# Kernel optimization log

Measured on AMD Instinct MI355X. Metric: run time of the kernel, lower is better.

Reference implementation:

```python
import jax, jax.numpy as jnp
from jax import lax
import numpy as np

B, S_DEC, S_ENC = 32, 128, 128
V, E, H = 32000, 200, 128


def setup_inputs() -> dict:
    key = jax.random.key(0)
    ks = jax.random.split(key, 10)
    emb = jax.random.normal(ks[0], (V, E), dtype=jnp.float32)
    emb = emb.at[0].set(0.0)  # padding_idx row (char2id[' '] -> 0)
    return {
        "sequence": jax.random.randint(ks[1], (B, S_DEC), 0, V),
        "hs": jax.random.normal(ks[2], (B, S_ENC, H), dtype=jnp.float32),
        "h": jax.random.normal(ks[3], (1, B, H), dtype=jnp.float32),
        "emb": emb,
        "w_ih": jax.random.normal(ks[4], (3 * H, E), dtype=jnp.float32) * 0.05,
        "w_hh": jax.random.normal(ks[5], (3 * H, H), dtype=jnp.float32) * 0.05,
        "b_ih": jax.random.normal(ks[6], (3 * H,), dtype=jnp.float32) * 0.05,
        "b_hh": jax.random.normal(ks[7], (3 * H,), dtype=jnp.float32) * 0.05,
        "w_out": jax.random.normal(ks[8], (V, 2 * H), dtype=jnp.float32) * 0.05,
        "b_out": jax.random.normal(ks[9], (V,), dtype=jnp.float32) * 0.05,
    }


def _gru(x_gates, h0, w_hh, b_hh):
    # x_gates: [B, S, 3H] precomputed input projections; torch gate order r,z,n
    def step(hprev, xg):
        hg = hprev @ w_hh.T + b_hh
        xr, xz, xn = jnp.split(xg, 3, axis=-1)
        hr, hz, hn = jnp.split(hg, 3, axis=-1)
        r = jax.nn.sigmoid(xr + hr)
        z = jax.nn.sigmoid(xz + hz)
        n = jnp.tanh(xn + r * hn)
        hnew = (1.0 - z) * n + z * hprev
        return hnew, hnew

    hT, outs = lax.scan(step, h0, jnp.swapaxes(x_gates, 0, 1))  # scan over time
    return jnp.swapaxes(outs, 0, 1), hT  # [B,S,H], [B,H]


def reference(sequence, hs, h, emb, w_ih, w_hh, b_ih, b_hh, w_out, b_out):
    # Embedding lookup (padding row already zero)
    x = emb[sequence]  # [B, S_dec, E]
    x_gates = jnp.einsum("bse,ge->bsg", x, w_ih) + b_ih  # [B, S_dec, 3H]
    output, hT = _gru(x_gates, h[0], w_hh, b_hh)  # [B, S_dec, H]
    state = hT[None]  # [1, B, H]
    # s = bmm(hs, output^T): [B, S_enc, S_dec]; softmax over encoder axis (dim=1)
    s = jnp.einsum("beh,bdh->bed", hs, output)
    attention_weight = jax.nn.softmax(s, axis=1)
    # context: replaces the per-timestep python loop with one contraction
    c = jnp.einsum("bed,beh->bdh", attention_weight, hs)  # [B, S_dec, H]
    cat = jnp.concatenate([output, c], axis=-1)  # [B, S_dec, 2H]
    logits = jnp.einsum("bdh,vh->bdv", cat, w_out) + b_out  # [B, S_dec, V]
    return logits, state, attention_weight
```

## Files before the change

kernel.cpp:

```cpp
#include <hip/hip_runtime.h>
#include <hip/hip_bf16.h>

#define B_    32
#define SDEC  128
#define SENC  128
#define V_    32000
#define E_    200
#define H_    128
#define G3    384

typedef __attribute__((ext_vector_type(8))) short bf16x8;
typedef __attribute__((ext_vector_type(4))) float f32x4;
typedef __attribute__((ext_vector_type(2))) float f32x2;

#define GLOBAL_AS __attribute__((address_space(1)))
#define LDS_AS    __attribute__((address_space(3)))

__device__ __forceinline__ float fast_sigmoid(float x) {
  return 1.f / (1.f + __expf(-x));
}
__device__ __forceinline__ float fast_tanh(float x) {
  float e2 = __expf(2.f * x);
  return 1.f - 2.f / (e2 + 1.f);
}

__global__ __launch_bounds__(192) void k_embed_proj(
    const int* __restrict__ seq, const float* __restrict__ emb,
    const float* __restrict__ w_ih, const float* __restrict__ b_ih,
    float* __restrict__ xg) {
  __shared__ __align__(16) float xs[16][E_];
  __shared__ int sidx[16];
  const int r0 = blockIdx.x * 16;
  const int t = threadIdx.x;
  if (t < 16) sidx[t] = seq[r0 + t];
  __syncthreads();
  for (int i = t; i < 800; i += 192) {
    int r = i / 50, c = i - r * 50;
    *(float4*)&xs[r][c * 4] =
        *(const float4*)(emb + (size_t)sidx[r] * E_ + c * 4);
  }
  __syncthreads();
  const int g0 = t, g1 = t + 192;
  float a0[16], a1[16];
#pragma unroll
  for (int r = 0; r < 16; r++) { a0[r] = 0.f; a1[r] = 0.f; }
  const float* w0 = w_ih + (size_t)g0 * E_;
  const float* w1 = w_ih + (size_t)g1 * E_;
  for (int k = 0; k < E_; k += 4) {
    float4 wv0 = *(const float4*)(w0 + k);
    float4 wv1 = *(const float4*)(w1 + k);
#pragma unroll
    for (int r = 0; r < 16; r++) {
      float4 xv = *(const float4*)&xs[r][k];
      a0[r] += wv0.x * xv.x + wv0.y * xv.y + wv0.z * xv.z + wv0.w * xv.w;
      a1[r] += wv1.x * xv.x + wv1.y * xv.y + wv1.z * xv.z + wv1.w * xv.w;
    }
  }
  const float b0 = b_ih[g0], b1 = b_ih[g1];
#pragma unroll
  for (int r = 0; r < 16; r++) {
    xg[(size_t)(r0 + r) * G3 + g0] = a0[r] + b0;
    xg[(size_t)(r0 + r) * G3 + g1] = a1[r] + b1;
  }
}

__global__ __launch_bounds__(512) void k_gru_cvt(
    const float* __restrict__ xg, const float* __restrict__ h0,
    const float* __restrict__ w_hh, const float* __restrict__ b_hh,
    __hip_bfloat16* __restrict__ cat_bf, float* __restrict__ state_out,
    const float* __restrict__ w_out, __hip_bfloat16* __restrict__ wout_bf) {
  if (blockIdx.x >= 32) {
    int idx = ((blockIdx.x - 32) * 512 + threadIdx.x) * 8;
    float4 a = *(const float4*)(w_out + idx);
    float4 c = *(const float4*)(w_out + idx + 4);
    union { __hip_bfloat16 h[8]; uint4 v; } p;
    p.h[0] = __float2bfloat16(a.x); p.h[1] = __float2bfloat16(a.y);
    p.h[2] = __float2bfloat16(a.z); p.h[3] = __float2bfloat16(a.w);
    p.h[4] = __float2bfloat16(c.x); p.h[5] = __float2bfloat16(c.y);
    p.h[6] = __float2bfloat16(c.z); p.h[7] = __float2bfloat16(c.w);
    *(uint4*)(wout_bf + idx) = p.v;
    return;
  }

  const int b = blockIdx.x;
  const int t = threadIdx.x;
  const int hh = t >> 2;
  const int sub = t & 3;

  float wr_[32], wz_[32], wn_[32];
#pragma unroll
  for (int m = 0; m < 8; m++) {
    int c = (m + sub * 2) & 7;
    int kb = sub * 32 + c * 4;
    *(float4*)&wr_[m * 4] = *(const float4*)(w_hh + (size_t)hh * H_ + kb);
    *(float4*)&wz_[m * 4] = *(const float4*)(w_hh + (size_t)(128 + hh) * H_ + kb);
    *(float4*)&wn_[m * 4] = *(const float4*)(w_hh + (size_t)(256 + hh) * H_ + kb);
  }

  __shared__ __align__(16) float hp[2][H_];
  const float* xgb = xg + (size_t)b * SDEC * G3;
  const float br = b_hh[hh], bz = b_hh[128 + hh], bn = b_hh[256 + hh];
  float cxr = xgb[hh], cxz = xgb[128 + hh], cxn = xgb[256 + hh];
  if (t < H_) hp[0][t] = h0[b * H_ + t];
  __hip_bfloat16* catbfb = cat_bf + (size_t)b * SDEC * 256;
  __syncthreads();

  int cur = 0;
  for (int s = 0; s < SDEC; s++) {
    float nxr = 0.f, nxz = 0.f, nxn = 0.f;
    if (s + 1 < SDEC) {
      const float* xp = xgb + (size_t)(s + 1) * G3;
      nxr = xp[hh]; nxz = xp[128 + hh]; nxn = xp[256 + hh];
    }
    f32x2 sr2 = {0.f, 0.f}, sz2 = {0.f, 0.f}, sn2 = {0.f, 0.f};
#pragma unroll
    for (int m = 0; m < 8; m++) {
      int c = (m + sub * 2) & 7;
      float4 hv = *(const float4*)&hp[cur][sub * 32 + c * 4];
      f32x2 h01 = {hv.x, hv.y}, h23 = {hv.z, hv.w};
      const f32x2* w2r = (const f32x2*)&wr_[m * 4];
      const f32x2* w2z = (const f32x2*)&wz_[m * 4];
      const f32x2* w2n = (const f32x2*)&wn_[m * 4];
      sr2 += w2r[0] * h01; sr2 += w2r[1] * h23;
      sz2 += w2z[0] * h01; sz2 += w2z[1] * h23;
      sn2 += w2n[0] * h01; sn2 += w2n[1] * h23;
    }
    float sr = sr2[0] + sr2[1];
    float sz = sz2[0] + sz2[1];
    float sn = sn2[0] + sn2[1];
    sr += __shfl_xor(sr, 1); sr += __shfl_xor(sr, 2);
    sz += __shfl_xor(sz, 1); sz += __shfl_xor(sz, 2);
    sn += __shfl_xor(sn, 1); sn += __shfl_xor(sn, 2);

    float hold = hp[cur][hh];
    float r = fast_sigmoid(cxr + sr + br);
    float z = fast_sigmoid(cxz + sz + bz);
    float n = fast_tanh(cxn + r * (sn + bn));
    float hnew = (1.f - z) * n + z * hold;
    if (sub == 0) {
      hp[cur ^ 1][hh] = hnew;
      catbfb[(size_t)s * 256 + hh] = __float2bfloat16(hnew);
    }
    __syncthreads();
    cur ^= 1;
    cxr = nxr; cxz = nxz; cxn = nxn;
  }
  if (t < H_) state_out[b * H_ + t] = hp[cur][t];
}

__global__ __launch_bounds__(512) void k_attn_mfma(
    const float* __restrict__ hs, __hip_bfloat16* __restrict__ cat_bf,
    float* __restrict__ attw_out) {
  __shared__ __hip_bfloat16 hsb[128][128];
  __shared__ __hip_bfloat16 hsT[128][128];
  __shared__ __hip_bfloat16 ctb[128][128];
  __shared__ __hip_bfloat16 plds[128][128];
  const int b = blockIdx.x;
  const int t = threadIdx.x;
  const int w = t >> 6, l = t & 63;
  const int lr = l & 15, lk = l >> 4;
  const float* hsbase = hs + (size_t)b * SENC * H_;

  for (int i = t; i < 2048; i += 512) {
    int d = i >> 4, c = i & 15;
    uint4 v = *(const uint4*)(cat_bf + (size_t)(b * SDEC + d) * 256 + c * 8);
    *(uint4*)&ctb[d][((c ^ (d & 7)) * 8)] = v;
  }
  for (int i = t; i < 2048; i += 512) {
    int e = i >> 4, c = i & 15;
    float4 v0 = *(const float4*)(hsbase + e * H_ + c * 8);
    float4 v1 = *(const float4*)(hsbase + e * H_ + c * 8 + 4);
    union { __hip_bfloat16 h[8]; uint4 u; } pk;
    pk.h[0] = __float2bfloat16(v0.x); pk.h[1] = __float2bfloat16(v0.y);
    pk.h[2] = __float2bfloat16(v0.z); pk.h[3] = __float2bfloat16(v0.w);
    pk.h[4] = __float2bfloat16(v1.x); pk.h[5] = __float2bfloat16(v1.y);
    pk.h[6] = __float2bfloat16(v1.z); pk.h[7] = __float2bfloat16(v1.w);
    *(uint4*)&hsb[e][((c ^ (e & 7)) * 8)] = pk.u;
  }
  __syncthreads();

  for (int i = t; i < 2048; i += 512) {
    int c = i >> 7, e = i & 127;
    uint4 v = *(const uint4*)&hsb[e][((c ^ (e & 7)) * 8)];
    const __hip_bfloat16* hv = (const __hip_bfloat16*)&v;
#pragma unroll
    for (int u = 0; u < 8; u++) {
      int h = c * 8 + u;
      int col = (e + 8 * (h & 15)) & 127;
      hsT[h][col] = hv[u];
    }
  }
  __syncthreads();

  f32x4 acc[8];
#pragma unroll
  for (int et = 0; et < 8; et++) acc[et] = (f32x4){0.f, 0.f, 0.f, 0.f};
  bf16x8 afrag[4];
#pragma unroll
  for (int kt = 0; kt < 4; kt++)
    afrag[kt] = *(const bf16x8*)&ctb[w * 16 + lr][(((kt * 4 + lk) ^ (lr & 7)) * 8)];
#pragma unroll
  for (int et = 0; et < 8; et++) {
#pragma unroll
    for (int kt = 0; kt < 4; kt++) {
      bf16x8 bfrag =
          *(const bf16x8*)&hsb[et * 16 + lr][(((kt * 4 + lk) ^ (lr & 7)) * 8)];
      acc[et] =
          __builtin_amdgcn_mfma_f32_16x16x32_bf16(bfrag, afrag[kt], acc[et], 0, 0, 0);
    }
  }

  float mx = -1e30f;
#pragma unroll
  for (int et = 0; et < 8; et++) {
    mx = fmaxf(mx, fmaxf(fmaxf(acc[et][0], acc[et][1]),
                         fmaxf(acc[et][2], acc[et][3])));
  }
  mx = fmaxf(mx, __shfl_xor(mx, 16));
  mx = fmaxf(mx, __shfl_xor(mx, 32));
  float sum = 0.f;
#pragma unroll
  for (int et = 0; et < 8; et++) {
    acc[et][0] = __expf(acc[et][0] - mx);
    acc[et][1] = __expf(acc[et][1] - mx);
    acc[et][2] = __expf(acc[et][2] - mx);
    acc[et][3] = __expf(acc[et][3] - mx);
    sum += acc[et][0] + acc[et][1] + acc[et][2] + acc[et][3];
  }
  sum += __shfl_xor(sum, 16);
  sum += __shfl_xor(sum, 32);
  const float inv = 1.f / sum;

  const int d = w * 16 + lr;
  float* aw = attw_out + (size_t)b * SENC * SDEC + d;
#pragma unroll
  for (int et = 0; et < 8; et++) {
    acc[et][0] *= inv; acc[et][1] *= inv;
    acc[et][2] *= inv; acc[et][3] *= inv;
    union { __hip_bfloat16 h[4]; uint2 u; } pk4;
    pk4.h[0] = __float2bfloat16(acc[et][0]);
    pk4.h[1] = __float2bfloat16(acc[et][1]);
    pk4.h[2] = __float2bfloat16(acc[et][2]);
    pk4.h[3] = __float2bfloat16(acc[et][3]);
    *(uint2*)&plds[d][(((et * 2 + (lk >> 1)) ^ (lr & 7)) * 8 + 4 * (lk & 1))] =
        pk4.u;
    const int e0 = et * 16 + lk * 4;
#pragma unroll
    for (int j = 0; j < 4; j++)
      aw[(size_t)(e0 + j) * SDEC] = acc[et][j];
  }
  __syncthreads();

  bf16x8 pfrag[4];
#pragma unroll
  for (int f = 0; f < 4; f++)
    pfrag[f] = *(const bf16x8*)&plds[d][(((f * 4 + lk) ^ (lr & 7)) * 8)];
#pragma unroll
  for (int ht = 0; ht < 8; ht++) {
    f32x4 a2 = (f32x4){0.f, 0.f, 0.f, 0.f};
#pragma unroll
    for (int kt = 0; kt < 4; kt++) {
      bf16x8 hfrag =
          *(const bf16x8*)&hsT[ht * 16 + lr][((kt * 32 + lk * 8 + 8 * lr) & 127)];
      a2 = __builtin_amdgcn_mfma_f32_16x16x32_bf16(hfrag, pfrag[kt], a2, 0, 0, 0);
    }
    union { __hip_bfloat16 h[4]; uint2 u; } pk4;
    pk4.h[0] = __float2bfloat16(a2[0]);
    pk4.h[1] = __float2bfloat16(a2[1]);
    pk4.h[2] = __float2bfloat16(a2[2]);
    pk4.h[3] = __float2bfloat16(a2[3]);
    *(uint2*)(cat_bf + (size_t)(b * SDEC + d) * 256 + 128 + ht * 16 + lk * 4) =
        pk4.u;
  }
}

__global__ __launch_bounds__(512) void k_gemm_mfma(
    const __hip_bfloat16* __restrict__ A, const __hip_bfloat16* __restrict__ Bw,
    const float* __restrict__ b_out, float* __restrict__ C) {
  constexpr int K = 256, N = V_, Kt = 32;
  alignas(16) __shared__ char smem[73728];
  __hip_bfloat16 (*As)[4096] = (__hip_bfloat16(*)[4096])smem;
  __hip_bfloat16 (*Bs)[8192] = (__hip_bfloat16(*)[8192])(smem + 24576);
  float* tr = (float*)smem;

  const int tid = threadIdx.x;
  const int w = tid >> 6, l = tid & 63;
  const int wr = w >> 2, wc = w & 3;
  const int lr = l & 15, lk = l >> 4;
  const int lq = l >> 2, lc = l & 3;

  const int bid = blockIdx.x;
  const int wgid = (bid & 7) * 500 + (bid >> 3);
  const int mt = wgid & 31;
  const int nt = wgid >> 5;
  const int m0 = mt * 128, n0 = nt * 256;

  f32x4 acc[4][4];
#pragma unroll
  for (int m = 0; m < 4; m++)
#pragma unroll
    for (int n = 0; n < 4; n++) acc[m][n] = (f32x4){0.f, 0.f, 0.f, 0.f};

#define STAGE(buf, kk)                                                            \
  do {                                                                            \
    const __hip_bfloat16* gA = A + (size_t)(m0 + w * 16 + lq) * K + (kk) + lc * 8;\
    const __hip_bfloat16* gB0 = Bw + (size_t)(n0 + w * 32 + lq) * K + (kk) + lc * 8;\
    const __hip_bfloat16* gB1 = gB0 + (size_t)16 * K;                             \
    __builtin_amdgcn_global_load_lds((const GLOBAL_AS void*)gA,                   \
        (LDS_AS void*)(&As[buf][w * 512]), 16, 0, 0);                             \
    __builtin_amdgcn_global_load_lds((const GLOBAL_AS void*)gB0,                  \
        (LDS_AS void*)(&Bs[buf][w * 1024]), 16, 0, 0);                            \
    __builtin_amdgcn_global_load_lds((const GLOBAL_AS void*)gB1,                  \
        (LDS_AS void*)(&Bs[buf][w * 1024 + 512]), 16, 0, 0);                      \
  } while (0)

  STAGE(0, 0);
  STAGE(1, Kt);

#pragma unroll
  for (int t = 0; t < 8; ++t) {
    if (t < 7) asm volatile("s_waitcnt vmcnt(3)" ::: "memory");
    else       asm volatile("s_waitcnt vmcnt(0)" ::: "memory");
    __builtin_amdgcn_s_barrier();
    asm volatile("" ::: "memory");

    const int c = t % 3;
    bf16x8 af[4], bfr[4];
#pragma unroll
    for (int m = 0; m < 4; m++)
      af[m] = *(const bf16x8*)(const void*)(&As[c][(wr * 64 + m * 16 + lr) * Kt + lk * 8]);
#pragma unroll
    for (int n = 0; n < 4; n++)
      bfr[n] = *(const bf16x8*)(const void*)(&Bs[c][(wc * 64 + n * 16 + lr) * Kt + lk * 8]);

    if (t < 6) STAGE((t + 2) % 3, (t + 2) * Kt);

#pragma unroll
    for (int m = 0; m < 4; m++)
#pragma unroll
      for (int n = 0; n < 4; n++)
        acc[m][n] = __builtin_amdgcn_mfma_f32_16x16x32_bf16(bfr[n], af[m], acc[m][n], 0, 0, 0);
  }
#undef STAGE

  __syncthreads();
#pragma unroll
  for (int h = 0; h < 2; ++h) {
    if (wr == h) {
#pragma unroll
      for (int m = 0; m < 4; m++) {
#pragma unroll
        for (int n = 0; n < 4; n++) {
          const int row = m * 16 + lr;
          const int col = wc * 64 + n * 16 + lk * 4;
          const float4 bo = *(const float4*)(b_out + n0 + col);
          f32x4 v;
          v[0] = acc[m][n][0] + bo.x;
          v[1] = acc[m][n][1] + bo.y;
          v[2] = acc[m][n][2] + bo.z;
          v[3] = acc[m][n][3] + bo.w;
          *(f32x4*)&tr[row * 260 + col] = v;
        }
      }
    }
    __syncthreads();
#pragma unroll
    for (int i = 0; i < 8; ++i) {
      const int c2 = i * 512 + tid;
      const int row = c2 >> 6;
      const int off = (c2 & 63) * 4;
      f32x4 v = *(const f32x4*)&tr[row * 260 + off];
      __builtin_nontemporal_store(
          v, (f32x4*)(C + (size_t)(m0 + h * 64 + row) * N + n0 + off));
    }
    __syncthreads();
  }
}

extern "C" void kernel_launch(void* const* d_in, const int* in_sizes, int n_in,
                              void* d_out, int out_size, void* d_ws, size_t ws_size,
                              hipStream_t stream) {
  const int* seq = (const int*)d_in[0];
  const float* hs = (const float*)d_in[1];
  const float* h0 = (const float*)d_in[2];
  const float* emb = (const float*)d_in[3];
  const float* w_ih = (const float*)d_in[4];
  const float* w_hh = (const float*)d_in[5];
  const float* b_ih = (const float*)d_in[6];
  const float* b_hh = (const float*)d_in[7];
  const float* w_out = (const float*)d_in[8];
  const float* b_out = (const float*)d_in[9];

  float* out = (float*)d_out;
  float* logits = out;
  float* state = out + 131072000;
  float* attw = out + 131072000 + 4096;

  char* ws = (char*)d_ws;
  float* xg = (float*)ws;
  __hip_bfloat16* cat_bf = (__hip_bfloat16*)(ws + 10485760);
  __hip_bfloat16* wout_bf = (__hip_bfloat16*)(ws + 12582912);

  k_embed_proj<<<256, 192, 0, stream>>>(seq, emb, w_ih, b_ih, xg);
  k_gru_cvt<<<2032, 512, 0, stream>>>(xg, h0, w_hh, b_hh, cat_bf, state,
                                      w_out, wout_bf);
  k_attn_mfma<<<32, 512, 0, stream>>>(hs, cat_bf, attw);
  k_gemm_mfma<<<4000, 512, 0, stream>>>(cat_bf, wout_bf, b_out, logits);
}
```

Baseline: 252.2 us.

## Fuse attention into GRU kernel and use DPP quad reductions with lighter barriers

Merges the attention kernel into the GRU recurrence kernel, so each batch block writes its hidden states straight into an LDS tile and then runs the attention MFMA and softmax without a separate launch or a reload of cat_bf. The per-step shuffle reductions are replaced with DPP quad_perm moves, and __syncthreads is replaced by an explicit lgkmcnt wait plus s_barrier. The P tile reuses the ctb LDS buffer to save space. In exchange, the fused kernel needs more LDS per block, which may lower occupancy for the w_out conversion blocks that share the launch, and the explicit barrier skips waiting on vmcnt.

```diff
diff --git a/kernel.cpp b/kernel.cpp
--- a/kernel.cpp
+++ b/kernel.cpp
@@ -22,6 +22,14 @@
 __device__ __forceinline__ float fast_tanh(float x) {
   float e2 = __expf(2.f * x);
   return 1.f - 2.f / (e2 + 1.f);
+}
+__device__ __forceinline__ float quad_reduce(float x) {
+  int i = __builtin_bit_cast(int, x);
+  int a = __builtin_amdgcn_mov_dpp(i, 0xB1, 0xF, 0xF, true);
+  float s = x + __builtin_bit_cast(float, a);
+  int j = __builtin_bit_cast(int, s);
+  int c = __builtin_amdgcn_mov_dpp(j, 0x4E, 0xF, 0xF, true);
+  return s + __builtin_bit_cast(float, c);
 }
 
 __global__ __launch_bounds__(192) void k_embed_proj(
@@ -64,10 +72,11 @@
   }
 }
 
-__global__ __launch_bounds__(512) void k_gru_cvt(
+__global__ __launch_bounds__(512) void k_gru_attn_cvt(
     const float* __restrict__ xg, const float* __restrict__ h0,
     const float* __restrict__ w_hh, const float* __restrict__ b_hh,
-    __hip_bfloat16* __restrict__ cat_bf, float* __restrict__ state_out,
+    const float* __restrict__ hs, __hip_bfloat16* __restrict__ cat_bf,
+    float* __restrict__ state_out, float* __restrict__ attw_out,
     const float* __restrict__ w_out, __hip_bfloat16* __restrict__ wout_bf) {
   if (blockIdx.x >= 32) {
     int idx = ((blockIdx.x - 32) * 512 + threadIdx.x) * 8;
@@ -82,6 +91,11 @@
     return;
   }
 
+  __shared__ __hip_bfloat16 ctb[128][128];
+  __shared__ __hip_bfloat16 hsb[128][128];
+  __shared__ __hip_bfloat16 hsT[128][128];
+  __shared__ __align__(16) float hp[2][H_];
+
   const int b = blockIdx.x;
   const int t = threadIdx.x;
   const int hh = t >> 2;
@@ -97,13 +111,15 @@
     *(float4*)&wn_[m * 4] = *(const float4*)(w_hh + (size_t)(256 + hh) * H_ + kb);
   }
 
-  __shared__ __align__(16) float hp[2][H_];
   const float* xgb = xg + (size_t)b * SDEC * G3;
   const float br = b_hh[hh], bz = b_hh[128 + hh], bn = b_hh[256 + hh];
   float cxr = xgb[hh], cxz = xgb[128 + hh], cxn = xgb[256 + hh];
   if (t < H_) hp[0][t] = h0[b * H_ + t];
   __hip_bfloat16* catbfb = cat_bf + (size_t)b * SDEC * 256;
-  __syncthreads();
+
+  asm volatile("s_waitcnt lgkmcnt(0)" ::: "memory");
+  __builtin_amdgcn_s_barrier();
+  asm volatile("" ::: "memory");
 
   int cur = 0;
   for (int s = 0; s < SDEC; s++) {
@@ -125,12 +141,9 @@
       sz2 += w2z[0] * h01; sz2 += w2z[1] * h23;
       sn2 += w2n[0] * h01; sn2 += w2n[1] * h23;
     }
-    float sr = sr2[0] + sr2[1];
-    float sz = sz2[0] + sz2[1];
-    float sn = sn2[0] + sn2[1];
-    sr += __shfl_xor(sr, 1); sr += __shfl_xor(sr, 2);
-    sz += __shfl_xor(sz, 1); sz += __shfl_xor(sz, 2);
-    sn += __shfl_xor(sn, 1); sn += __shfl_xor(sn, 2);
+    float sr = quad_reduce(sr2[0] + sr2[1]);
+    float sz = quad_reduce(sz2[0] + sz2[1]);
+    float sn = quad_reduce(sn2[0] + sn2[1]);
 
     float hold = hp[cur][hh];
     float r = fast_sigmoid(cxr + sr + br);
@@ -138,34 +151,22 @@
     float n = fast_tanh(cxn + r * (sn + bn));
     float hnew = (1.f - z) * n + z * hold;
     if (sub == 0) {
+      __hip_bfloat16 hb = __float2bfloat16(hnew);
       hp[cur ^ 1][hh] = hnew;
-      catbfb[(size_t)s * 256 + hh] = __float2bfloat16(hnew);
-    }
-    __syncthreads();
+      catbfb[(size_t)s * 256 + hh] = hb;
+      ctb[s][((hh >> 3) ^ (s & 7)) * 8 + (hh & 7)] = hb;
+    }
+    asm volatile("s_waitcnt lgkmcnt(0)" ::: "memory");
+    __builtin_amdgcn_s_barrier();
+    asm volatile("" ::: "memory");
     cur ^= 1;
     cxr = nxr; cxz = nxz; cxn = nxn;
   }
-  if (t < H_) state_out[b * H_ + t] = hp[cur][t];
-}
-
-__global__ __launch_bounds__(512) void k_attn_mfma(
-    const float* __restrict__ hs, __hip_bfloat16* __restrict__ cat_bf,
-    float* __restrict__ attw_out) {
-  __shared__ __hip_bfloat16 hsb[128][128];
-  __shared__ __hip_bfloat16 hsT[128][128];
-  __shared__ __hip_bfloat16 ctb[128][128];
-  __shared__ __hip_bfloat16 plds[128][128];
-  const int b = blockIdx.x;
-  const int t = threadIdx.x;
+
   const int w = t >> 6, l = t & 63;
   const int lr = l & 15, lk = l >> 4;
   const float* hsbase = hs + (size_t)b * SENC * H_;
 
-  for (int i = t; i < 2048; i += 512) {
-    int d = i >> 4, c = i & 15;
-    uint4 v = *(const uint4*)(cat_bf + (size_t)(b * SDEC + d) * 256 + c * 8);
-    *(uint4*)&ctb[d][((c ^ (d & 7)) * 8)] = v;
-  }
   for (int i = t; i < 2048; i += 512) {
     int e = i >> 4, c = i & 15;
     float4 v0 = *(const float4*)(hsbase + e * H_ + c * 8);
@@ -177,6 +178,7 @@
     pk.h[6] = __float2bfloat16(v1.z); pk.h[7] = __float2bfloat16(v1.w);
     *(uint4*)&hsb[e][((c ^ (e & 7)) * 8)] = pk.u;
   }
+  if (t < H_) state_out[b * H_ + t] = hp[cur][t];
   __syncthreads();
 
   for (int i = t; i < 2048; i += 512) {
@@ -190,15 +192,16 @@
       hsT[h][col] = hv[u];
     }
   }
+  const int d = w * 16 + lr;
+  bf16x8 afrag[4];
+#pragma unroll
+  for (int kt = 0; kt < 4; kt++)
+    afrag[kt] = *(const bf16x8*)&ctb[d][(((kt * 4 + lk) ^ (lr & 7)) * 8)];
   __syncthreads();
 
   f32x4 acc[8];
 #pragma unroll
   for (int et = 0; et < 8; et++) acc[et] = (f32x4){0.f, 0.f, 0.f, 0.f};
-  bf16x8 afrag[4];
-#pragma unroll
-  for (int kt = 0; kt < 4; kt++)
-    afrag[kt] = *(const bf16x8*)&ctb[w * 16 + lr][(((kt * 4 + lk) ^ (lr & 7)) * 8)];
 #pragma unroll
   for (int et = 0; et < 8; et++) {
 #pragma unroll
@@ -212,10 +215,9 @@
 
   float mx = -1e30f;
 #pragma unroll
-  for (int et = 0; et < 8; et++) {
+  for (int et = 0; et < 8; et++)
     mx = fmaxf(mx, fmaxf(fmaxf(acc[et][0], acc[et][1]),
                          fmaxf(acc[et][2], acc[et][3])));
-  }
   mx = fmaxf(mx, __shfl_xor(mx, 16));
   mx = fmaxf(mx, __shfl_xor(mx, 32));
   float sum = 0.f;
@@ -231,7 +233,7 @@
   sum += __shfl_xor(sum, 32);
   const float inv = 1.f / sum;
 
-  const int d = w * 16 + lr;
+  __hip_bfloat16 (*plds)[128] = ctb;
   float* aw = attw_out + (size_t)b * SENC * SDEC + d;
 #pragma unroll
   for (int et = 0; et < 8; et++) {
@@ -402,8 +404,7 @@
   __hip_bfloat16* wout_bf = (__hip_bfloat16*)(ws + 12582912);
 
   k_embed_proj<<<256, 192, 0, stream>>>(seq, emb, w_ih, b_ih, xg);
-  k_gru_cvt<<<2032, 512, 0, stream>>>(xg, h0, w_hh, b_hh, cat_bf, state,
-                                      w_out, wout_bf);
-  k_attn_mfma<<<32, 512, 0, stream>>>(hs, cat_bf, attw);
+  k_gru_attn_cvt<<<2032, 512, 0, stream>>>(xg, h0, w_hh, b_hh, hs, cat_bf,
+                                           state, attw, w_out, wout_bf);
   k_gemm_mfma<<<4000, 512, 0, stream>>>(cat_bf, wout_bf, b_out, logits);
 }
```

Result: no change. 251.8 us (-0.1%).

## Run GRU recurrence in one block with bf16 MFMA and split hi/lo hidden state

Applied to the files above, without the earlier changes.

Replaces the per-batch GRU blocks (32 blocks of 512 threads doing fp32 dot products) with a single 256-thread block. That block computes the hidden-to-hidden matmul for all 32 batches with bf16 MFMA, keeping W_hh fragments in registers. The hidden state is split into bf16 high and low parts to keep roughly fp32 accuracy, but W_hh is rounded to bf16, which adds error that compounds over the recurrence. The w_out conversion blocks now each process 8 chunks, the block count drops to 501, and the logits GEMM raises wave priority around its MFMA loop. The serial GRU chain now runs on one CU and depends on fewer, larger matrix ops per step instead of parallel per-batch blocks.

```diff
diff --git a/kernel.cpp b/kernel.cpp
--- a/kernel.cpp
+++ b/kernel.cpp
@@ -11,7 +11,6 @@
 
 typedef __attribute__((ext_vector_type(8))) short bf16x8;
 typedef __attribute__((ext_vector_type(4))) float f32x4;
-typedef __attribute__((ext_vector_type(2))) float f32x2;
 
 #define GLOBAL_AS __attribute__((address_space(1)))
 #define LDS_AS    __attribute__((address_space(3)))
@@ -64,88 +63,164 @@
   }
 }
 
-__global__ __launch_bounds__(512) void k_gru_cvt(
+__global__ __launch_bounds__(256) void k_gru_mfma_cvt(
     const float* __restrict__ xg, const float* __restrict__ h0,
     const float* __restrict__ w_hh, const float* __restrict__ b_hh,
     __hip_bfloat16* __restrict__ cat_bf, float* __restrict__ state_out,
     const float* __restrict__ w_out, __hip_bfloat16* __restrict__ wout_bf) {
-  if (blockIdx.x >= 32) {
-    int idx = ((blockIdx.x - 32) * 512 + threadIdx.x) * 8;
-    float4 a = *(const float4*)(w_out + idx);
-    float4 c = *(const float4*)(w_out + idx + 4);
-    union { __hip_bfloat16 h[8]; uint4 v; } p;
-    p.h[0] = __float2bfloat16(a.x); p.h[1] = __float2bfloat16(a.y);
-    p.h[2] = __float2bfloat16(a.z); p.h[3] = __float2bfloat16(a.w);
-    p.h[4] = __float2bfloat16(c.x); p.h[5] = __float2bfloat16(c.y);
-    p.h[6] = __float2bfloat16(c.z); p.h[7] = __float2bfloat16(c.w);
-    *(uint4*)(wout_bf + idx) = p.v;
+  if (blockIdx.x >= 1) {
+    const size_t base = (size_t)(blockIdx.x - 1) * 16384;
+#pragma unroll
+    for (int j = 0; j < 8; j++) {
+      size_t idx = base + (size_t)j * 2048 + (size_t)threadIdx.x * 8;
+      float4 a = *(const float4*)(w_out + idx);
+      float4 c = *(const float4*)(w_out + idx + 4);
+      union { __hip_bfloat16 h[8]; uint4 v; } p;
+      p.h[0] = __float2bfloat16(a.x); p.h[1] = __float2bfloat16(a.y);
+      p.h[2] = __float2bfloat16(a.z); p.h[3] = __float2bfloat16(a.w);
+      p.h[4] = __float2bfloat16(c.x); p.h[5] = __float2bfloat16(c.y);
+      p.h[6] = __float2bfloat16(c.z); p.h[7] = __float2bfloat16(c.w);
+      *(uint4*)(wout_bf + idx) = p.v;
+    }
     return;
   }
 
-  const int b = blockIdx.x;
+  __shared__ ushort Hh[2][32][136];
+  __shared__ ushort Hl[2][32][136];
+
   const int t = threadIdx.x;
-  const int hh = t >> 2;
-  const int sub = t & 3;
-
-  float wr_[32], wz_[32], wn_[32];
-#pragma unroll
-  for (int m = 0; m < 8; m++) {
-    int c = (m + sub * 2) & 7;
-    int kb = sub * 32 + c * 4;
-    *(float4*)&wr_[m * 4] = *(const float4*)(w_hh + (size_t)hh * H_ + kb);
-    *(float4*)&wz_[m * 4] = *(const float4*)(w_hh + (size_t)(128 + hh) * H_ + kb);
-    *(float4*)&wn_[m * 4] = *(const float4*)(w_hh + (size_t)(256 + hh) * H_ + kb);
-  }
-
-  __shared__ __align__(16) float hp[2][H_];
-  const float* xgb = xg + (size_t)b * SDEC * G3;
-  const float br = b_hh[hh], bz = b_hh[128 + hh], bn = b_hh[256 + hh];
-  float cxr = xgb[hh], cxz = xgb[128 + hh], cxn = xgb[256 + hh];
-  if (t < H_) hp[0][t] = h0[b * H_ + t];
-  __hip_bfloat16* catbfb = cat_bf + (size_t)b * SDEC * 256;
-  __syncthreads();
+  const int w4 = t >> 6, l = t & 63;
+  const int lr = l & 15, lk = l >> 4;
+
+  bf16x8 Wf[3][2][4];
+#pragma unroll
+  for (int g = 0; g < 3; g++)
+#pragma unroll
+    for (int ht2 = 0; ht2 < 2; ht2++)
+#pragma unroll
+      for (int kt = 0; kt < 4; kt++) {
+        const float* wp = w_hh +
+            (size_t)(g * 128 + (w4 + ht2 * 4) * 16 + lr) * H_ + kt * 32 + lk * 8;
+        float4 a = *(const float4*)wp;
+        float4 c = *(const float4*)(wp + 4);
+        union { __hip_bfloat16 h[8]; bf16x8 v; } pk;
+        pk.h[0] = __float2bfloat16(a.x); pk.h[1] = __float2bfloat16(a.y);
+        pk.h[2] = __float2bfloat16(a.z); pk.h[3] = __float2bfloat16(a.w);
+        pk.h[4] = __float2bfloat16(c.x); pk.h[5] = __float2bfloat16(c.y);
+        pk.h[6] = __float2bfloat16(c.z); pk.h[7] = __float2bfloat16(c.w);
+        Wf[g][ht2][kt] = pk.v;
+      }
+
+  f32x4 bb[3][2];
+#pragma unroll
+  for (int g = 0; g < 3; g++)
+#pragma unroll
+    for (int ht2 = 0; ht2 < 2; ht2++)
+      bb[g][ht2] = *(const f32x4*)(b_hh + g * 128 + (w4 + ht2 * 4) * 16 + lk * 4);
+
+  float hp_[2][2][4];
+#pragma unroll
+  for (int ht2 = 0; ht2 < 2; ht2++)
+#pragma unroll
+    for (int bt = 0; bt < 2; bt++) {
+      const int b = bt * 16 + lr;
+      const int hhb = (w4 + ht2 * 4) * 16 + lk * 4;
+      f32x4 h4 = *(const f32x4*)(h0 + (size_t)b * H_ + hhb);
+      union { __hip_bfloat16 h[4]; uint2 u; } hi, lo;
+#pragma unroll
+      for (int j = 0; j < 4; j++) {
+        float v = h4[j];
+        hp_[ht2][bt][j] = v;
+        __hip_bfloat16 hb = __float2bfloat16(v);
+        hi.h[j] = hb;
+        lo.h[j] = __float2bfloat16(v - (float)hb);
+      }
+      *(uint2*)&Hh[0][b][hhb] = hi.u;
+      *(uint2*)&Hl[0][b][hhb] = lo.u;
+    }
+  asm volatile("s_waitcnt lgkmcnt(0)" ::: "memory");
+  __builtin_amdgcn_s_barrier();
+  asm volatile("" ::: "memory");
 
   int cur = 0;
   for (int s = 0; s < SDEC; s++) {
-    float nxr = 0.f, nxz = 0.f, nxn = 0.f;
-    if (s + 1 < SDEC) {
-      const float* xp = xgb + (size_t)(s + 1) * G3;
-      nxr = xp[hh]; nxz = xp[128 + hh]; nxn = xp[256 + hh];
-    }
-    f32x2 sr2 = {0.f, 0.f}, sz2 = {0.f, 0.f}, sn2 = {0.f, 0.f};
-#pragma unroll
-    for (int m = 0; m < 8; m++) {
-      int c = (m + sub * 2) & 7;
-      float4 hv = *(const float4*)&hp[cur][sub * 32 + c * 4];
-      f32x2 h01 = {hv.x, hv.y}, h23 = {hv.z, hv.w};
-      const f32x2* w2r = (const f32x2*)&wr_[m * 4];
-      const f32x2* w2z = (const f32x2*)&wz_[m * 4];
-      const f32x2* w2n = (const f32x2*)&wn_[m * 4];
-      sr2 += w2r[0] * h01; sr2 += w2r[1] * h23;
-      sz2 += w2z[0] * h01; sz2 += w2z[1] * h23;
-      sn2 += w2n[0] * h01; sn2 += w2n[1] * h23;
-    }
-    float sr = sr2[0] + sr2[1];
-    float sz = sz2[0] + sz2[1];
-    float sn = sn2[0] + sn2[1];
-    sr += __shfl_xor(sr, 1); sr += __shfl_xor(sr, 2);
-    sz += __shfl_xor(sz, 1); sz += __shfl_xor(sz, 2);
-    sn += __shfl_xor(sn, 1); sn += __shfl_xor(sn, 2);
-
-    float hold = hp[cur][hh];
-    float r = fast_sigmoid(cxr + sr + br);
-    float z = fast_sigmoid(cxz + sz + bz);
-    float n = fast_tanh(cxn + r * (sn + bn));
-    float hnew = (1.f - z) * n + z * hold;
-    if (sub == 0) {
-      hp[cur ^ 1][hh] = hnew;
-      catbfb[(size_t)s * 256 + hh] = __float2bfloat16(hnew);
-    }
-    __syncthreads();
+    f32x4 xgl[3][2][2];
+#pragma unroll
+    for (int g = 0; g < 3; g++)
+#pragma unroll
+      for (int ht2 = 0; ht2 < 2; ht2++)
+#pragma unroll
+        for (int bt = 0; bt < 2; bt++) {
+          const int b = bt * 16 + lr;
+          xgl[g][ht2][bt] = *(const f32x4*)(xg +
+              (size_t)(b * SDEC + s) * G3 + g * 128 + (w4 + ht2 * 4) * 16 + lk * 4);
+        }
+
+    bf16x8 Fh[2][4], Fl[2][4];
+#pragma unroll
+    for (int bt = 0; bt < 2; bt++)
+#pragma unroll
+      for (int kt = 0; kt < 4; kt++) {
+        const int b = bt * 16 + lr;
+        Fh[bt][kt] = *(const bf16x8*)&Hh[cur][b][kt * 32 + lk * 8];
+        Fl[bt][kt] = *(const bf16x8*)&Hl[cur][b][kt * 32 + lk * 8];
+      }
+
+    f32x4 acc[3][2][2];
+#pragma unroll
+    for (int g = 0; g < 3; g++)
+#pragma unroll
+      for (int ht2 = 0; ht2 < 2; ht2++)
+#pragma unroll
+        for (int bt = 0; bt < 2; bt++) {
+          f32x4 a2 = (f32x4){0.f, 0.f, 0.f, 0.f};
+#pragma unroll
+          for (int kt = 0; kt < 4; kt++) {
+            a2 = __builtin_amdgcn_mfma_f32_16x16x32_bf16(Wf[g][ht2][kt], Fh[bt][kt], a2, 0, 0, 0);
+            a2 = __builtin_amdgcn_mfma_f32_16x16x32_bf16(Wf[g][ht2][kt], Fl[bt][kt], a2, 0, 0, 0);
+          }
+          acc[g][ht2][bt] = a2;
+        }
+
+#pragma unroll
+    for (int ht2 = 0; ht2 < 2; ht2++)
+#pragma unroll
+      for (int bt = 0; bt < 2; bt++) {
+        const int b = bt * 16 + lr;
+        const int hhb = (w4 + ht2 * 4) * 16 + lk * 4;
+        union { __hip_bfloat16 h[4]; uint2 u; } hi, lo;
+#pragma unroll
+        for (int j = 0; j < 4; j++) {
+          float r = fast_sigmoid(xgl[0][ht2][bt][j] + acc[0][ht2][bt][j] + bb[0][ht2][j]);
+          float z = fast_sigmoid(xgl[1][ht2][bt][j] + acc[1][ht2][bt][j] + bb[1][ht2][j]);
+          float n = fast_tanh(xgl[2][ht2][bt][j] + r * (acc[2][ht2][bt][j] + bb[2][ht2][j]));
+          float hnew = (1.f - z) * n + z * hp_[ht2][bt][j];
+          hp_[ht2][bt][j] = hnew;
+          __hip_bfloat16 hb = __float2bfloat16(hnew);
+          hi.h[j] = hb;
+          lo.h[j] = __float2bfloat16(hnew - (float)hb);
+        }
+        *(uint2*)(cat_bf + (size_t)(b * SDEC + s) * 256 + hhb) = hi.u;
+        *(uint2*)&Hh[cur ^ 1][b][hhb] = hi.u;
+        *(uint2*)&Hl[cur ^ 1][b][hhb] = lo.u;
+      }
+    asm volatile("s_waitcnt lgkmcnt(0)" ::: "memory");
+    __builtin_amdgcn_s_barrier();
+    asm volatile("" ::: "memory");
     cur ^= 1;
-    cxr = nxr; cxz = nxz; cxn = nxn;
-  }
-  if (t < H_) state_out[b * H_ + t] = hp[cur][t];
+  }
+
+#pragma unroll
+  for (int ht2 = 0; ht2 < 2; ht2++)
+#pragma unroll
+    for (int bt = 0; bt < 2; bt++) {
+      const int b = bt * 16 + lr;
+      const int hhb = (w4 + ht2 * 4) * 16 + lk * 4;
+      f32x4 v;
+      v[0] = hp_[ht2][bt][0]; v[1] = hp_[ht2][bt][1];
+      v[2] = hp_[ht2][bt][2]; v[3] = hp_[ht2][bt][3];
+      *(f32x4*)(state_out + (size_t)b * H_ + hhb) = v;
+    }
 }
 
 __global__ __launch_bounds__(512) void k_attn_mfma(
@@ -212,10 +287,9 @@
 
   float mx = -1e30f;
 #pragma unroll
-  for (int et = 0; et < 8; et++) {
+  for (int et = 0; et < 8; et++)
     mx = fmaxf(mx, fmaxf(fmaxf(acc[et][0], acc[et][1]),
                          fmaxf(acc[et][2], acc[et][3])));
-  }
   mx = fmaxf(mx, __shfl_xor(mx, 16));
   mx = fmaxf(mx, __shfl_xor(mx, 32));
   float sum = 0.f;
@@ -335,11 +409,13 @@
 
     if (t < 6) STAGE((t + 2) % 3, (t + 2) * Kt);
 
+    __builtin_amdgcn_s_setprio(1);
 #pragma unroll
     for (int m = 0; m < 4; m++)
 #pragma unroll
       for (int n = 0; n < 4; n++)
         acc[m][n] = __builtin_amdgcn_mfma_f32_16x16x32_bf16(bfr[n], af[m], acc[m][n], 0, 0, 0);
+    __builtin_amdgcn_s_setprio(0);
   }
 #undef STAGE
 
@@ -402,8 +478,8 @@
   __hip_bfloat16* wout_bf = (__hip_bfloat16*)(ws + 12582912);
 
   k_embed_proj<<<256, 192, 0, stream>>>(seq, emb, w_ih, b_ih, xg);
-  k_gru_cvt<<<2032, 512, 0, stream>>>(xg, h0, w_hh, b_hh, cat_bf, state,
-                                      w_out, wout_bf);
+  k_gru_mfma_cvt<<<501, 256, 0, stream>>>(xg, h0, w_hh, b_hh, cat_bf, state,
+                                          w_out, wout_bf);
   k_attn_mfma<<<32, 512, 0, stream>>>(hs, cat_bf, attw);
   k_gemm_mfma<<<4000, 512, 0, stream>>>(cat_bf, wout_bf, b_out, logits);
 }
```

Result: slower. 759.6 us (+201.2%).
